# Kernel optimization log

Hardware: AMD Instinct MI355X
Metric: run time of the kernel (lower is better)

## Reference

```python
import jax, jax.numpy as jnp
import numpy as np

B, N_C, N_T, D, DF = 16, 2048, 1024, 2, 2
K, E_OBS = 16, 4
H, DH = 4, 16
F = H * DH  # 64-dim node features (embed_all output)


def setup_inputs() -> dict:
    key = jax.random.key(0)
    ks = jax.random.split(key, 16)
    r = lambda i, shape: jax.random.normal(ks[i], shape, jnp.float32) * 0.05
    d_in = E_OBS + D + DF  # obs(4) + s(2) + f(2) = 8
    return dict(
        s_ctx=jax.random.normal(ks[0], (B, N_C, D), jnp.float32),
        f_ctx=jax.random.normal(ks[1], (B, N_C, DF), jnp.float32),
        s_test=jax.random.normal(ks[2], (B, N_T, D), jnp.float32),
        emb_obs=r(3, (2, E_OBS)),
        W1=r(4, (d_in, 256)), b1=jnp.zeros((256,), jnp.float32),
        W2=r(5, (256, 128)), b2=jnp.zeros((128,), jnp.float32),
        W3=r(6, (128, F)), b3=jnp.zeros((F,), jnp.float32),
        ln_g=jnp.ones((F,), jnp.float32), ln_b=jnp.zeros((F,), jnp.float32),
        Wg=r(7, (F, F)),
        a_src=r(8, (H, DH)), a_dst=r(9, (H, DH)),
        We=r(10, (D, H)), be=jnp.zeros((H,), jnp.float32),
        H1=r(11, (F, 256)), c1=jnp.zeros((256,), jnp.float32),
        H2=r(12, (256, 64)), c2=jnp.zeros((64,), jnp.float32),
        H3=r(13, (64, 2)), c3=jnp.zeros((2,), jnp.float32),
    )


def _knn(q, ctx, k):
    # q [B,Nq,D], ctx [B,Nc,D] -> neighbor indices [B,Nq,K] and displacement edge feats [B,Nq,K,D]
    d2 = (jnp.sum(q * q, -1)[:, :, None] + jnp.sum(ctx * ctx, -1)[:, None, :]
          - 2.0 * jnp.einsum('bqd,bcd->bqc', q, ctx))
    _, idx = jax.lax.top_k(-d2, k)
    nb = jax.vmap(lambda c, i: c[i])(ctx, idx)  # gather neighbor coords per batch
    return idx, q[:, :, None, :] - nb


def _mlp3(x, W1, b1, W2, b2, W3, b3):
    x = jax.nn.gelu(x @ W1 + b1)
    x = jax.nn.gelu(x @ W2 + b2)
    return x @ W3 + b3


def _ln(x, g, b):
    mu = jnp.mean(x, -1, keepdims=True)
    v = jnp.var(x, -1, keepdims=True)
    return (x - mu) * jax.lax.rsqrt(v + 1e-6) * g + b


def reference(s_ctx, f_ctx, s_test, emb_obs, W1, b1, W2, b2, W3, b3, ln_g, ln_b,
              Wg, a_src, a_dst, We, be, H1, c1, H2, c2, H3, c3):
    # --- build kNN graph (ctx->ctx and ctx->test edges, K per receiver) ---
    s_cc, d_cc = _knn(s_ctx, s_ctx, K)
    s_ct, d_ct = _knn(s_test, s_ctx, K)
    edges = jnp.concatenate([d_cc.reshape(-1, D), d_ct.reshape(-1, D)], axis=0)  # [E, D]
    off = (jnp.arange(B) * N_C)[:, None, None]
    senders = jnp.concatenate([(s_cc + off).reshape(-1), (s_ct + off).reshape(-1)])  # [E]
    # receivers == repeat(arange(N), K): edges are grouped K-per-node in node order.

    # --- node embedding: [obs_embed | s | f] -> MLP -> LayerNorm ---
    ctx_in = jnp.concatenate([jnp.broadcast_to(emb_obs[1], (B, N_C, E_OBS)), s_ctx, f_ctx], -1)
    test_in = jnp.concatenate([jnp.broadcast_to(emb_obs[0], (B, N_T, E_OBS)), s_test,
                               jnp.zeros((B, N_T, DF), s_test.dtype)], -1)
    n_ctx = _ln(_mlp3(ctx_in, W1, b1, W2, b2, W3, b3), ln_g, ln_b)
    n_test = _ln(_mlp3(test_in, W1, b1, W2, b2, W3, b3), ln_g, ln_b)
    nodes = jnp.concatenate([n_ctx.reshape(B * N_C, F), n_test.reshape(B * N_T, F)], 0)
    N = B * (N_C + N_T)

    # --- edge-biased GAT message passing (K incoming edges per node) ---
    xp = (nodes @ Wg).reshape(N, H, DH)
    msg = xp[senders].reshape(N, K, H, DH)  # gather sender features
    sc = (jnp.einsum('nkhd,hd->nkh', msg, a_src)
          + jnp.einsum('nhd,hd->nh', xp, a_dst)[:, None, :])
    sc = jax.nn.leaky_relu(sc, 0.2) + (edges @ We + be).reshape(N, K, H)  # edge bias
    alpha = jax.nn.softmax(sc, axis=1)  # softmax over the K neighbors
    out = jnp.einsum('nkh,nkhd->nhd', alpha, msg).reshape(N, F)
    nodes = nodes + out  # residual

    # --- head on test nodes + diagonal MVN output ---
    n_t = nodes[-B * N_T:].reshape(B, N_T, F)
    o = jax.nn.gelu(n_t @ H1 + c1)
    o = jax.nn.gelu(o @ H2 + c2)
    o = o @ H3 + c3  # [B, N_t, 2]
    mean = o[..., 0:1]
    scale = jax.nn.softplus(o[..., 1:2])
    return jnp.concatenate([mean, scale], -1)
```

## Files before the change

kernel.cpp:

```cpp
#include <hip/hip_runtime.h>
#include <math.h>

#define NB 16
#define NCTX 2048
#define NTEST 1024
#define NCTX_TOT (NB*NCTX)
#define NTEST_TOT (NB*NTEST)
#define NTOT (NCTX_TOT + NTEST_TOT)

typedef _Float16 half8 __attribute__((ext_vector_type(8)));
typedef _Float16 half4 __attribute__((ext_vector_type(4)));
typedef float f32x4 __attribute__((ext_vector_type(4)));

__device__ __forceinline__ float gelu_f(float x) {
  float x3 = x * x * x;
  float y = 0.7978845608028654f * fmaf(0.044715f, x3, x);
  float e = __expf(2.0f * y);
  float th = 1.0f - 2.0f * __builtin_amdgcn_rcpf(e + 1.0f);
  return 0.5f * x * (1.0f + th);
}

__device__ __forceinline__ void fma4(float4& a, float s, float4 w) {
  a.x = fmaf(s, w.x, a.x);
  a.y = fmaf(s, w.y, a.y);
  a.z = fmaf(s, w.z, a.z);
  a.w = fmaf(s, w.w, a.w);
}

__device__ __forceinline__ float4 ldg4(const float* p) {
  return *reinterpret_cast<const float4*>(p);
}

__device__ __forceinline__ unsigned fkey(float f) {
  unsigned u = __float_as_uint(f);
  return (u & 0x80000000u) ? ~u : (u ^ 0x80000000u);
}
__device__ __forceinline__ float unfkey(unsigned k) {
  return (k & 0x80000000u) ? __uint_as_float(k ^ 0x80000000u)
                           : __uint_as_float(~k);
}

__global__ __launch_bounds__(256, 3) void knn_prep_kernel(
    const float* __restrict__ s_ctx, const float* __restrict__ s_test,
    int* __restrict__ senders,
    const float* __restrict__ W1, const float* __restrict__ b1,
    const float* __restrict__ emb,
    const float* __restrict__ W2, const float* __restrict__ W3,
    const float* __restrict__ Wg,
    const float* __restrict__ H1, const float* __restrict__ H2,
    _Float16* __restrict__ W2P, _Float16* __restrict__ W3P,
    _Float16* __restrict__ WgP,
    _Float16* __restrict__ H1P, _Float16* __restrict__ H2P,
    float* __restrict__ ctype)
{
  __shared__ __align__(16) unsigned long long sk[4][128];
  const int blk = blockIdx.x;

  if (blk < 40) {
    const int t = blk*256 + (int)threadIdx.x;
    if (t < 4096) {
      int i = t;
      int j = i >> 9, ks = (i >> 6) & 7, l = i & 63;
      int col = 16*j + (l & 15);
      int k0  = ks*32 + (l >> 4)*8;
      half8 o;
      #pragma unroll
      for (int e = 0; e < 8; ++e) o[e] = (_Float16)W2[(k0 + e)*128 + col];
      *reinterpret_cast<half8*>(&W2P[(size_t)i*8]) = o;
    } else if (t < 5120) {
      int i = t - 4096;
      int j = i >> 8, ks = (i >> 6) & 3, l = i & 63;
      int col = 16*j + (l & 15);
      int k0  = ks*32 + (l >> 4)*8;
      half8 o;
      #pragma unroll
      for (int e = 0; e < 8; ++e) o[e] = (_Float16)W3[(k0 + e)*64 + col];
      *reinterpret_cast<half8*>(&W3P[(size_t)i*8]) = o;
    } else if (t < 5632) {
      int i = t - 5120;
      int j = i >> 7, ks = (i >> 6) & 1, l = i & 63;
      int col = 16*j + (l & 15);
      int k0  = ks*32 + (l >> 4)*8;
      half8 o;
      #pragma unroll
      for (int e = 0; e < 8; ++e) o[e] = (_Float16)Wg[(k0 + e)*64 + col];
      *reinterpret_cast<half8*>(&WgP[(size_t)i*8]) = o;
    } else if (t < 7680) {
      int i = t - 5632;
      int j = i >> 7, ks = (i >> 6) & 1, l = i & 63;
      int col = 16*j + (l & 15);
      int k0  = ks*32 + (l >> 4)*8;
      half8 o;
      #pragma unroll
      for (int e = 0; e < 8; ++e) o[e] = (_Float16)H1[(k0 + e)*256 + col];
      *reinterpret_cast<half8*>(&H1P[(size_t)i*8]) = o;
    } else if (t < 9728) {
      int i = t - 7680;
      int j = i >> 9, ks = (i >> 6) & 7, l = i & 63;
      int col = 16*j + (l & 15);
      int k0  = ks*32 + (l >> 4)*8;
      half8 o;
      #pragma unroll
      for (int e = 0; e < 8; ++e) o[e] = (_Float16)H2[(k0 + e)*64 + col];
      *reinterpret_cast<half8*>(&H2P[(size_t)i*8]) = o;
    } else {
      int i = t - 9728;
      int ty = i >> 8, c = i & 255;
      float acc = b1[c];
      #pragma unroll
      for (int k = 0; k < 4; ++k) acc = fmaf(emb[ty*4 + k], W1[k*256 + c], acc);
      ctype[i] = acc;
    }
    return;
  }

  const int t    = threadIdx.x;
  const int lane = t & 63;
  const int w    = t >> 6;
  const int b0   = blk - 40;
  const int unit = (b0 & 7)*512 + (b0 >> 3);
  const int bb   = unit >> 8;
  const int q    = (unit & 255) * 4 + w;
  const int trow = bb * NTEST + q;

  const float* cb = s_ctx + (size_t)bb * NCTX * 2;
  const float qx = s_test[(size_t)trow*2];
  const float qy = s_test[(size_t)trow*2 + 1];
  const float qq = __fadd_rn(__fmul_rn(qx,qx), __fmul_rn(qy,qy));

  float2 p[32];
  #pragma unroll
  for (int it = 0; it < 32; ++it)
    p[it] = *reinterpret_cast<const float2*>(&cb[2*(it*64 + lane)]);

  float d[32];
  float mn = 3.4e38f;
  #pragma unroll
  for (int it = 0; it < 32; ++it) {
    float ss  = __fadd_rn(__fmul_rn(p[it].x,p[it].x), __fmul_rn(p[it].y,p[it].y));
    float dot = __fadd_rn(__fmul_rn(qx, p[it].x), __fmul_rn(qy, p[it].y));
    float d2  = __fsub_rn(__fadd_rn(qq, ss), __fmul_rn(2.0f, dot));
    d[it] = d2;
    mn = fminf(mn, d2);
  }

  unsigned v = fkey(mn);
  #pragma unroll
  for (int k = 2; k <= 64; k <<= 1) {
    #pragma unroll
    for (int j = k >> 1; j >= 1; j >>= 1) {
      unsigned pv = (unsigned)__shfl_xor((int)v, j);
      bool up      = ((lane & k) == 0);
      bool lowHalf = ((lane & j) == 0);
      bool keepMin = (lowHalf == up);
      unsigned mnv = v < pv ? v : pv;
      unsigned mxv = v < pv ? pv : v;
      v = keepMin ? mnv : mxv;
    }
  }
  const float Tf = unfkey((unsigned)__shfl((int)v, 15));

  int cnt = 0;
  #pragma unroll
  for (int it = 0; it < 32; ++it) cnt += (int)(d[it] <= Tf);
  int inc = cnt;
  #pragma unroll
  for (int o = 1; o < 64; o <<= 1) {
    int y = __shfl_up(inc, o);
    if (lane >= o) inc += y;
  }
  const int S = __shfl(inc, 63);
  int pos = inc - cnt;
  #pragma unroll
  for (int it = 0; it < 32; ++it) {
    if (d[it] <= Tf) {
      if (pos < 128)
        sk[w][pos] = ((unsigned long long)fkey(d[it]) << 32)
                   | (unsigned)(it*64 + lane);
      ++pos;
    }
  }

  if (S <= 32) {
    if (lane >= S && lane < 32) sk[w][lane] = ~0ULL;
    unsigned long long pm = sk[w][lane & 31];
    unsigned long long kv[32];
    #pragma unroll
    for (int j = 0; j < 32; ++j) kv[j] = sk[w][j];
    int r0 = 0;
    #pragma unroll
    for (int j = 0; j < 32; ++j)
      r0 += (int)(kv[j] < pm);
    if (lane < S && r0 < 16)
      senders[(size_t)trow*16 + r0] = bb*NCTX + (int)(pm & 0xFFFFFFFFu);
  } else if (S <= 128) {
    unsigned long long p0 = (lane      < S) ? sk[w][lane]      : ~0ULL;
    unsigned long long p1 = (lane + 64 < S) ? sk[w][lane + 64] : ~0ULL;
    int r0 = 0, r1 = 0;
    for (int j = 0; j < S; ++j) {
      unsigned long long kj = sk[w][j];
      r0 += (int)(kj < p0);
      r1 += (int)(kj < p1);
    }
    if (lane < S && r0 < 16)
      senders[(size_t)trow*16 + r0] = bb*NCTX + (int)(p0 & 0xFFFFFFFFu);
    if (lane + 64 < S && r1 < 16)
      senders[(size_t)trow*16 + r1] = bb*NCTX + (int)(p1 & 0xFFFFFFFFu);
  } else {
    if (lane == 0) {
      float dist[16]; int ind[16];
      #pragma unroll
      for (int j=0;j<16;++j){ dist[j]=3.4e38f; ind[j]=0; }
      for (int c = 0; c < NCTX; ++c) {
        float2 pp = *reinterpret_cast<const float2*>(&cb[2*c]);
        float ss  = __fadd_rn(__fmul_rn(pp.x,pp.x), __fmul_rn(pp.y,pp.y));
        float dot = __fadd_rn(__fmul_rn(qx, pp.x), __fmul_rn(qy, pp.y));
        float d2  = __fsub_rn(__fadd_rn(qq, ss), __fmul_rn(2.0f, dot));
        if (d2 < dist[15]) {
          float dj = d2; int ij = c;
          #pragma unroll
          for (int j = 0; j < 16; ++j) {
            bool sw = dj < dist[j];
            float td = dist[j]; int ti = ind[j];
            dist[j] = sw ? dj : td;  ind[j] = sw ? ij : ti;
            dj = sw ? td : dj;       ij = sw ? ti : ij;
          }
        }
      }
      for (int j = 0; j < 16; ++j)
        senders[(size_t)trow*16 + j] = bb*NCTX + ind[j];
    }
  }
}

__global__ __launch_bounds__(256, 4) void mlp_kernel(
    const float* __restrict__ s_ctx, const float* __restrict__ f_ctx,
    const float* __restrict__ s_test,
    const float* __restrict__ ctype, const float* __restrict__ W1,
    const _Float16* __restrict__ W2P, const float* __restrict__ b2,
    const _Float16* __restrict__ W3P, const float* __restrict__ b3,
    const float* __restrict__ ln_g, const float* __restrict__ ln_b,
    const _Float16* __restrict__ WgP,
    const float* __restrict__ a_src, const float* __restrict__ a_dst,
    float* __restrict__ nodes, _Float16* __restrict__ xph,
    float* __restrict__ xps, float* __restrict__ xpd)
{
  __shared__ __align__(16) char smem[34816];
  const int t    = threadIdx.x;
  const int lane = t & 63;
  const int w    = t >> 6;
  const int id   = blockIdx.x;
  char* slice = smem + w * 8704;
  _Float16* h1t  = reinterpret_cast<_Float16*>(slice);
  float (*xin)[4] = reinterpret_cast<float(*)[4]>(slice + 8448);
  _Float16* h2   = h1t;
  _Float16* nodh = h1t + 16*136;
  const int cn = lane & 15;
  const int kg = lane >> 4;
  const int m0 = (id*4 + w) * 16;
  const bool is_ctx = (m0 < NCTX_TOT);

  const _Float16* bQ2 = W2P + lane*8;
  const _Float16* bQ3 = W3P + lane*8;
  const _Float16* bQg = WgP + lane*8;

  half8 bb2[8];
  #pragma unroll
  for (int j = 0; j < 8; ++j)
    bb2[j] = *reinterpret_cast<const half8*>(bQ2 + j*4096);

  {
    int r = lane >> 2, c = lane & 3;
    int n = m0 + r;
    float v;
    if (is_ctx) v = (c < 2) ? s_ctx[2*(size_t)n + c] : f_ctx[2*(size_t)n + (c-2)];
    else { int tn = n - NCTX_TOT; v = (c < 2) ? s_test[2*(size_t)tn + c] : 0.f; }
    xin[r][c] = v;
  }

  {
    const int c0 = lane * 4;
    float4 w4 = ldg4(&W1[4*256 + c0]);
    float4 w5 = ldg4(&W1[5*256 + c0]);
    float4 w6 = ldg4(&W1[6*256 + c0]);
    float4 w7 = ldg4(&W1[7*256 + c0]);
    float4 cbv = ldg4(&ctype[(is_ctx ? 256 : 0) + c0]);
    #pragma unroll
    for (int r = 0; r < 16; ++r) {
      float4 xi = *reinterpret_cast<const float4*>(&xin[r][0]);
      float4 a = cbv;
      fma4(a, xi.x, w4); fma4(a, xi.y, w5);
      fma4(a, xi.z, w6); fma4(a, xi.w, w7);
      half4 o = { (_Float16)gelu_f(a.x), (_Float16)gelu_f(a.y),
                  (_Float16)gelu_f(a.z), (_Float16)gelu_f(a.w) };
      *reinterpret_cast<half4*>(&h1t[r*264 + c0]) = o;
    }
  }

  {
    f32x4 acc[8];
    #pragma unroll
    for (int j = 0; j < 8; ++j) {
      float bv = b2[16*j + cn];
      acc[j] = (f32x4){bv, bv, bv, bv};
    }
    const _Float16* aP = h1t + cn*264 + kg*8;
    #pragma unroll
    for (int ks = 0; ks < 8; ++ks) {
      half8 a = *reinterpret_cast<const half8*>(aP + ks*32);
      half8 bn[8];
      if (ks < 7) {
        #pragma unroll
        for (int j = 0; j < 8; ++j)
          bn[j] = *reinterpret_cast<const half8*>(bQ2 + j*4096 + (ks+1)*512);
      }
      #pragma unroll
      for (int j = 0; j < 8; ++j)
        acc[j] = __builtin_amdgcn_mfma_f32_16x16x32_f16(a, bb2[j], acc[j], 0, 0, 0);
      if (ks < 7) {
        #pragma unroll
        for (int j = 0; j < 8; ++j) bb2[j] = bn[j];
      }
    }
    #pragma unroll
    for (int j = 0; j < 8; ++j)
      #pragma unroll
      for (int r = 0; r < 4; ++r) {
        int m = kg*4 + r;
        h2[m*136 + 16*j + cn] = (_Float16)gelu_f(acc[j][r]);
      }
  }

  {
    f32x4 acc[4];
    #pragma unroll
    for (int j = 0; j < 4; ++j) {
      float bv = b3[16*j + cn];
      acc[j] = (f32x4){bv, bv, bv, bv};
    }
    const _Float16* aP = h2 + cn*136 + kg*8;
    half8 bb[4];
    #pragma unroll
    for (int j = 0; j < 4; ++j)
      bb[j] = *reinterpret_cast<const half8*>(bQ3 + j*2048);
    #pragma unroll
    for (int ks = 0; ks < 4; ++ks) {
      half8 a = *reinterpret_cast<const half8*>(aP + ks*32);
      half8 bn[4];
      if (ks < 3) {
        #pragma unroll
        for (int j = 0; j < 4; ++j)
          bn[j] = *reinterpret_cast<const half8*>(bQ3 + j*2048 + (ks+1)*512);
      }
      #pragma unroll
      for (int j = 0; j < 4; ++j)
        acc[j] = __builtin_amdgcn_mfma_f32_16x16x32_f16(a, bb[j], acc[j], 0, 0, 0);
      if (ks < 3) {
        #pragma unroll
        for (int j = 0; j < 4; ++j) bb[j] = bn[j];
      }
    }
    float gv[4], bvv[4];
    #pragma unroll
    for (int j = 0; j < 4; ++j) { gv[j] = ln_g[16*j+cn]; bvv[j] = ln_b[16*j+cn]; }
    const bool is_test = !is_ctx;
    #pragma unroll
    for (int r = 0; r < 4; ++r) {
      float sv = 0.f, sq = 0.f;
      #pragma unroll
      for (int j = 0; j < 4; ++j) {
        float v = acc[j][r];
        sv += v; sq += v*v;
      }
      #pragma unroll
      for (int o = 1; o < 16; o <<= 1) {
        sv += __shfl_xor(sv, o);
        sq += __shfl_xor(sq, o);
      }
      float mean = sv * (1.0f/64.0f);
      float var  = sq * (1.0f/64.0f) - mean*mean;
      float rstd = rsqrtf(var + 1e-6f);
      int m = kg*4 + r;
      #pragma unroll
      for (int j = 0; j < 4; ++j) {
        float v = (acc[j][r] - mean) * rstd * gv[j] + bvv[j];
        nodh[m*72 + 16*j + cn] = (_Float16)v;
        if (is_test)
          nodes[(size_t)(m0 + m)*64 + 16*j + cn] = v;
      }
    }
  }

  {
    f32x4 acc[4];
    #pragma unroll
    for (int j = 0; j < 4; ++j) acc[j] = (f32x4){0.f, 0.f, 0.f, 0.f};
    const _Float16* aP = nodh + cn*72 + kg*8;
    half8 bg0[4], bg1[4];
    #pragma unroll
    for (int j = 0; j < 4; ++j) {
      bg0[j] = *reinterpret_cast<const half8*>(bQg + j*1024);
      bg1[j] = *reinterpret_cast<const half8*>(bQg + j*1024 + 512);
    }
    half8 a0 = *reinterpret_cast<const half8*>(aP);
    half8 a1 = *reinterpret_cast<const half8*>(aP + 32);
    #pragma unroll
    for (int j = 0; j < 4; ++j)
      acc[j] = __builtin_amdgcn_mfma_f32_16x16x32_f16(a0, bg0[j], acc[j], 0, 0, 0);
    #pragma unroll
    for (int j = 0; j < 4; ++j)
      acc[j] = __builtin_amdgcn_mfma_f32_16x16x32_f16(a1, bg1[j], acc[j], 0, 0, 0);
    #pragma unroll
    for (int r = 0; r < 4; ++r) {
      int m = kg*4 + r;
      #pragma unroll
      for (int j = 0; j < 4; ++j)
        xph[(size_t)(m0 + m)*64 + 16*j + cn] = (_Float16)acc[j][r];
    }
    const float* av = is_ctx ? a_src : a_dst;
    float av0 = av[cn], av1 = av[16+cn], av2 = av[32+cn], av3 = av[48+cn];
    #pragma unroll
    for (int r = 0; r < 4; ++r) {
      float p0 = acc[0][r]*av0, p1 = acc[1][r]*av1;
      float p2 = acc[2][r]*av2, p3 = acc[3][r]*av3;
      #pragma unroll
      for (int o = 1; o < 16; o <<= 1) {
        p0 += __shfl_xor(p0, o); p1 += __shfl_xor(p1, o);
        p2 += __shfl_xor(p2, o); p3 += __shfl_xor(p3, o);
      }
      if (cn == 0) {
        int m = kg*4 + r;
        float4 v = make_float4(p0, p1, p2, p3);
        if (is_ctx)
          *reinterpret_cast<float4*>(&xps[(size_t)(m0 + m)*4]) = v;
        else
          *reinterpret_cast<float4*>(&xpd[(size_t)(m0 + m - NCTX_TOT)*4]) = v;
      }
    }
  }
}

__global__ __launch_bounds__(64, 3) void back_kernel(
    const float* __restrict__ s_ctx, const float* __restrict__ s_test,
    const _Float16* __restrict__ xph, const int* __restrict__ senders,
    const float* __restrict__ xps, const float* __restrict__ xpd,
    const float* __restrict__ We, const float* __restrict__ be,
    const float* __restrict__ nodes,
    const _Float16* __restrict__ H1P, const float* __restrict__ c1,
    const _Float16* __restrict__ H2P, const float* __restrict__ c2,
    const float* __restrict__ H3, const float* __restrict__ c3,
    float* __restrict__ outp)
{
  __shared__ __align__(16) _Float16 xinh[16*72];
  __shared__ __align__(16) _Float16 h1[16*264];
  const int lane = threadIdx.x;
  const int cn   = lane & 15;
  const int kg   = lane >> 4;
  const int bid  = blockIdx.x;
  const int L    = (bid & 7)*256 + (bid >> 3);
  const int row0 = L * 8;

  #pragma unroll
  for (int rr = 8; rr < 16; ++rr) xinh[rr*72 + lane] = (_Float16)0.f;

  {
    const int h  = kg;
    const int kk = cn;
    const int hb = lane & 48;
    const float we0 = We[h], we1 = We[4+h], beh = be[h];
    for (int rr = 0; rr < 8; ++rr) {
      const int trow = row0 + rr;
      int s = senders[(size_t)trow*16 + kk];
      s = (s < 0) ? 0 : ((s >= NCTX_TOT) ? NCTX_TOT - 1 : s);
      float pre = xps[(size_t)s*4 + h] + xpd[(size_t)trow*4 + h];
      float lr  = pre >= 0.f ? pre : 0.2f * pre;
      const float qx = s_test[(size_t)trow*2];
      const float qy = s_test[(size_t)trow*2 + 1];
      float ex = qx - s_ctx[(size_t)s*2];
      float ey = qy - s_ctx[(size_t)s*2 + 1];
      float sc = lr + fmaf(ex, we0, fmaf(ey, we1, beh));
      float mx = sc;
      #pragma unroll
      for (int o = 1; o < 16; o <<= 1) mx = fmaxf(mx, __shfl_xor(mx, o));
      float e = __expf(sc - mx);
      float sum = e;
      #pragma unroll
      for (int o = 1; o < 16; o <<= 1) sum += __shfl_xor(sum, o);
      float alpha = e / sum;
      float outv = 0.f;
      #pragma unroll
      for (int k = 0; k < 16; ++k) {
        int   sk = __shfl(s, k);
        float al = __shfl(alpha, hb + k);
        outv = fmaf(al, (float)xph[(size_t)sk*64 + lane], outv);
      }
      float xv = nodes[(size_t)(NCTX_TOT + trow)*64 + lane] + outv;
      xinh[rr*72 + lane] = (_Float16)xv;
    }
  }

  {
    const _Float16* aP  = xinh + cn*72 + kg*8;
    const _Float16* bQ1 = H1P + lane*8;
    half8 a0 = *reinterpret_cast<const half8*>(aP);
    half8 a1 = *reinterpret_cast<const half8*>(aP + 32);
    #pragma unroll
    for (int g = 0; g < 2; ++g) {
      f32x4 acc[8];
      #pragma unroll
      for (int j = 0; j < 8; ++j) {
        float bv = c1[16*(g*8 + j) + cn];
        acc[j] = (f32x4){bv, bv, bv, bv};
      }
      half8 b0[8], b1[8];
      #pragma unroll
      for (int j = 0; j < 8; ++j) {
        b0[j] = *reinterpret_cast<const half8*>(bQ1 + ((g*8 + j)*2 + 0)*512);
        b1[j] = *reinterpret_cast<const half8*>(bQ1 + ((g*8 + j)*2 + 1)*512);
      }
      #pragma unroll
      for (int j = 0; j < 8; ++j)
        acc[j] = __builtin_amdgcn_mfma_f32_16x16x32_f16(a0, b0[j], acc[j], 0, 0, 0);
      #pragma unroll
      for (int j = 0; j < 8; ++j)
        acc[j] = __builtin_amdgcn_mfma_f32_16x16x32_f16(a1, b1[j], acc[j], 0, 0, 0);
      #pragma unroll
      for (int j = 0; j < 8; ++j)
        #pragma unroll
        for (int r = 0; r < 4; ++r)
          h1[(kg*4 + r)*264 + 16*(g*8 + j) + cn] = (_Float16)gelu_f(acc[j][r]);
    }
  }

  {
    f32x4 acc[4];
    #pragma unroll
    for (int j = 0; j < 4; ++j) {
      float bv = c2[16*j + cn];
      acc[j] = (f32x4){bv, bv, bv, bv};
    }
    const _Float16* aP  = h1 + cn*264 + kg*8;
    const _Float16* bQ2 = H2P + lane*8;
    half8 bb[4];
    #pragma unroll
    for (int j = 0; j < 4; ++j)
      bb[j] = *reinterpret_cast<const half8*>(bQ2 + j*4096);
    #pragma unroll
    for (int ks = 0; ks < 8; ++ks) {
      half8 a = *reinterpret_cast<const half8*>(aP + ks*32);
      half8 bn[4];
      if (ks < 7) {
        #pragma unroll
        for (int j = 0; j < 4; ++j)
          bn[j] = *reinterpret_cast<const half8*>(bQ2 + j*4096 + (ks+1)*512);
      }
      #pragma unroll
      for (int j = 0; j < 4; ++j)
        acc[j] = __builtin_amdgcn_mfma_f32_16x16x32_f16(a, bb[j], acc[j], 0, 0, 0);
      if (ks < 7) {
        #pragma unroll
        for (int j = 0; j < 4; ++j) bb[j] = bn[j];
      }
    }
    float h30[4], h31[4];
    #pragma unroll
    for (int j = 0; j < 4; ++j) {
      h30[j] = H3[(16*j + cn)*2 + 0];
      h31[j] = H3[(16*j + cn)*2 + 1];
    }
    const float c30 = c3[0], c31 = c3[1];
    #pragma unroll
    for (int r = 0; r < 4; ++r) {
      float p0 = 0.f, p1 = 0.f;
      #pragma unroll
      for (int j = 0; j < 4; ++j) {
        float g = gelu_f(acc[j][r]);
        p0 = fmaf(g, h30[j], p0);
        p1 = fmaf(g, h31[j], p1);
      }
      #pragma unroll
      for (int o = 1; o < 16; o <<= 1) {
        p0 += __shfl_xor(p0, o);
        p1 += __shfl_xor(p1, o);
      }
      if (cn == 0 && kg < 2) {
        int row = row0 + kg*4 + r;
        float m = p0 + c30;
        float sa = p1 + c31;
        float sv = fmaxf(sa, 0.f) + log1pf(__expf(-fabsf(sa)));
        outp[(size_t)row*2 + 0] = m;
        outp[(size_t)row*2 + 1] = sv;
      }
    }
  }
}

extern "C" void kernel_launch(void* const* d_in, const int* in_sizes, int n_in,
                              void* d_out, int out_size, void* d_ws, size_t ws_size,
                              hipStream_t stream) {
  const float* s_ctx  = (const float*)d_in[0];
  const float* f_ctx  = (const float*)d_in[1];
  const float* s_test = (const float*)d_in[2];
  const float* emb    = (const float*)d_in[3];
  const float* W1 = (const float*)d_in[4];
  const float* b1 = (const float*)d_in[5];
  const float* W2 = (const float*)d_in[6];
  const float* b2 = (const float*)d_in[7];
  const float* W3 = (const float*)d_in[8];
  const float* b3 = (const float*)d_in[9];
  const float* ln_g = (const float*)d_in[10];
  const float* ln_b = (const float*)d_in[11];
  const float* Wg = (const float*)d_in[12];
  const float* a_src = (const float*)d_in[13];
  const float* a_dst = (const float*)d_in[14];
  const float* We = (const float*)d_in[15];
  const float* be = (const float*)d_in[16];
  const float* H1 = (const float*)d_in[17];
  const float* c1 = (const float*)d_in[18];
  const float* H2 = (const float*)d_in[19];
  const float* c2 = (const float*)d_in[20];
  const float* H3 = (const float*)d_in[21];
  const float* c3 = (const float*)d_in[22];

  float* nodes   = (float*)d_ws;
  _Float16* xph  = (_Float16*)(nodes + (size_t)NTOT*64);
  int*   senders = (int*)(xph + (size_t)NTOT*64);
  _Float16* W2P  = (_Float16*)(senders + (size_t)NTEST_TOT*16);
  _Float16* W3P  = W2P + 32768;
  _Float16* WgP  = W3P + 8192;
  _Float16* H1P  = WgP + 4096;
  _Float16* H2P  = H1P + 16384;
  float*   ctype = (float*)(H2P + 16384);
  float*   xps   = ctype + 512;
  float*   xpd   = xps + (size_t)NCTX_TOT*4;
  float* outp    = (float*)d_out;

  hipLaunchKernelGGL(knn_prep_kernel, dim3(4136), dim3(256), 0, stream,
                     s_ctx, s_test, senders,
                     W1, b1, emb, W2, W3, Wg, H1, H2,
                     W2P, W3P, WgP, H1P, H2P, ctype);
  hipLaunchKernelGGL(mlp_kernel, dim3(768), dim3(256), 0, stream,
                     s_ctx, f_ctx, s_test, ctype, W1,
                     W2P, b2, W3P, b3, ln_g, ln_b, WgP,
                     a_src, a_dst, nodes, xph, xps, xpd);
  hipLaunchKernelGGL(back_kernel, dim3(2048), dim3(64), 0, stream,
                     s_ctx, s_test, xph, senders, xps, xpd, We, be,
                     nodes, H1P, c1, H2P, c2, H3, c3, outp);
}
```

Baseline: 71.56 us.

## Split back_kernel head across two waves with 16 real rows per block

Result: faster. 64.07 us (-10.5%).

```diff
diff --git a/kernel.cpp b/kernel.cpp
--- a/kernel.cpp
+++ b/kernel.cpp
@@ -440,7 +440,7 @@
   }
 }
 
-__global__ __launch_bounds__(64, 3) void back_kernel(
+__global__ __launch_bounds__(128, 3) void back_kernel(
     const float* __restrict__ s_ctx, const float* __restrict__ s_test,
     const _Float16* __restrict__ xph, const int* __restrict__ senders,
     const float* __restrict__ xps, const float* __restrict__ xpd,
@@ -453,15 +453,15 @@
 {
   __shared__ __align__(16) _Float16 xinh[16*72];
   __shared__ __align__(16) _Float16 h1[16*264];
-  const int lane = threadIdx.x;
+  __shared__ float pp[2][16][2];
+  const int tid  = threadIdx.x;
+  const int lane = tid & 63;
+  const int wv   = tid >> 6;
   const int cn   = lane & 15;
   const int kg   = lane >> 4;
   const int bid  = blockIdx.x;
-  const int L    = (bid & 7)*256 + (bid >> 3);
-  const int row0 = L * 8;
-
-  #pragma unroll
-  for (int rr = 8; rr < 16; ++rr) xinh[rr*72 + lane] = (_Float16)0.f;
+  const int L    = (bid & 7)*128 + (bid >> 3);
+  const int row0 = L * 16;
 
   {
     const int h  = kg;
@@ -469,7 +469,8 @@
     const int hb = lane & 48;
     const float we0 = We[h], we1 = We[4+h], beh = be[h];
     for (int rr = 0; rr < 8; ++rr) {
-      const int trow = row0 + rr;
+      const int rl   = wv*8 + rr;
+      const int trow = row0 + rl;
       int s = senders[(size_t)trow*16 + kk];
       s = (s < 0) ? 0 : ((s >= NCTX_TOT) ? NCTX_TOT - 1 : s);
       float pre = xps[(size_t)s*4 + h] + xpd[(size_t)trow*4 + h];
@@ -495,103 +496,114 @@
         outv = fmaf(al, (float)xph[(size_t)sk*64 + lane], outv);
       }
       float xv = nodes[(size_t)(NCTX_TOT + trow)*64 + lane] + outv;
-      xinh[rr*72 + lane] = (_Float16)xv;
-    }
-  }
+      xinh[rl*72 + lane] = (_Float16)xv;
+    }
+  }
+
+  __syncthreads();
 
   {
     const _Float16* aP  = xinh + cn*72 + kg*8;
     const _Float16* bQ1 = H1P + lane*8;
     half8 a0 = *reinterpret_cast<const half8*>(aP);
     half8 a1 = *reinterpret_cast<const half8*>(aP + 32);
-    #pragma unroll
-    for (int g = 0; g < 2; ++g) {
-      f32x4 acc[8];
-      #pragma unroll
-      for (int j = 0; j < 8; ++j) {
-        float bv = c1[16*(g*8 + j) + cn];
-        acc[j] = (f32x4){bv, bv, bv, bv};
-      }
-      half8 b0[8], b1[8];
-      #pragma unroll
-      for (int j = 0; j < 8; ++j) {
-        b0[j] = *reinterpret_cast<const half8*>(bQ1 + ((g*8 + j)*2 + 0)*512);
-        b1[j] = *reinterpret_cast<const half8*>(bQ1 + ((g*8 + j)*2 + 1)*512);
-      }
-      #pragma unroll
-      for (int j = 0; j < 8; ++j)
-        acc[j] = __builtin_amdgcn_mfma_f32_16x16x32_f16(a0, b0[j], acc[j], 0, 0, 0);
-      #pragma unroll
-      for (int j = 0; j < 8; ++j)
-        acc[j] = __builtin_amdgcn_mfma_f32_16x16x32_f16(a1, b1[j], acc[j], 0, 0, 0);
-      #pragma unroll
-      for (int j = 0; j < 8; ++j)
-        #pragma unroll
-        for (int r = 0; r < 4; ++r)
-          h1[(kg*4 + r)*264 + 16*(g*8 + j) + cn] = (_Float16)gelu_f(acc[j][r]);
-    }
-  }
-
-  {
-    f32x4 acc[4];
-    #pragma unroll
-    for (int j = 0; j < 4; ++j) {
+    const int g = wv;
+    f32x4 acc[8];
+    #pragma unroll
+    for (int j = 0; j < 8; ++j) {
+      float bv = c1[16*(g*8 + j) + cn];
+      acc[j] = (f32x4){bv, bv, bv, bv};
+    }
+    half8 b0[8], b1[8];
+    #pragma unroll
+    for (int j = 0; j < 8; ++j) {
+      b0[j] = *reinterpret_cast<const half8*>(bQ1 + ((g*8 + j)*2 + 0)*512);
+      b1[j] = *reinterpret_cast<const half8*>(bQ1 + ((g*8 + j)*2 + 1)*512);
+    }
+    #pragma unroll
+    for (int j = 0; j < 8; ++j)
+      acc[j] = __builtin_amdgcn_mfma_f32_16x16x32_f16(a0, b0[j], acc[j], 0, 0, 0);
+    #pragma unroll
+    for (int j = 0; j < 8; ++j)
+      acc[j] = __builtin_amdgcn_mfma_f32_16x16x32_f16(a1, b1[j], acc[j], 0, 0, 0);
+    #pragma unroll
+    for (int j = 0; j < 8; ++j)
+      #pragma unroll
+      for (int r = 0; r < 4; ++r)
+        h1[(kg*4 + r)*264 + 16*(g*8 + j) + cn] = (_Float16)gelu_f(acc[j][r]);
+  }
+
+  __syncthreads();
+
+  {
+    f32x4 acc[2];
+    #pragma unroll
+    for (int j2 = 0; j2 < 2; ++j2) {
+      const int j = wv*2 + j2;
       float bv = c2[16*j + cn];
-      acc[j] = (f32x4){bv, bv, bv, bv};
+      acc[j2] = (f32x4){bv, bv, bv, bv};
     }
     const _Float16* aP  = h1 + cn*264 + kg*8;
     const _Float16* bQ2 = H2P + lane*8;
-    half8 bb[4];
-    #pragma unroll
-    for (int j = 0; j < 4; ++j)
-      bb[j] = *reinterpret_cast<const half8*>(bQ2 + j*4096);
+    half8 bb[2];
+    #pragma unroll
+    for (int j2 = 0; j2 < 2; ++j2)
+      bb[j2] = *reinterpret_cast<const half8*>(bQ2 + (wv*2 + j2)*4096);
     #pragma unroll
     for (int ks = 0; ks < 8; ++ks) {
       half8 a = *reinterpret_cast<const half8*>(aP + ks*32);
-      half8 bn[4];
+      half8 bn[2];
       if (ks < 7) {
         #pragma unroll
-        for (int j = 0; j < 4; ++j)
-          bn[j] = *reinterpret_cast<const half8*>(bQ2 + j*4096 + (ks+1)*512);
-      }
-      #pragma unroll
-      for (int j = 0; j < 4; ++j)
-        acc[j] = __builtin_amdgcn_mfma_f32_16x16x32_f16(a, bb[j], acc[j], 0, 0, 0);
+        for (int j2 = 0; j2 < 2; ++j2)
+          bn[j2] = *reinterpret_cast<const half8*>(bQ2 + (wv*2 + j2)*4096 + (ks+1)*512);
+      }
+      #pragma unroll
+      for (int j2 = 0; j2 < 2; ++j2)
+        acc[j2] = __builtin_amdgcn_mfma_f32_16x16x32_f16(a, bb[j2], acc[j2], 0, 0, 0);
       if (ks < 7) {
         #pragma unroll
-        for (int j = 0; j < 4; ++j) bb[j] = bn[j];
-      }
-    }
-    float h30[4], h31[4];
-    #pragma unroll
-    for (int j = 0; j < 4; ++j) {
-      h30[j] = H3[(16*j + cn)*2 + 0];
-      h31[j] = H3[(16*j + cn)*2 + 1];
-    }
-    const float c30 = c3[0], c31 = c3[1];
+        for (int j2 = 0; j2 < 2; ++j2) bb[j2] = bn[j2];
+      }
+    }
+    float h30[2], h31[2];
+    #pragma unroll
+    for (int j2 = 0; j2 < 2; ++j2) {
+      const int j = wv*2 + j2;
+      h30[j2] = H3[(16*j + cn)*2 + 0];
+      h31[j2] = H3[(16*j + cn)*2 + 1];
+    }
     #pragma unroll
     for (int r = 0; r < 4; ++r) {
       float p0 = 0.f, p1 = 0.f;
       #pragma unroll
-      for (int j = 0; j < 4; ++j) {
-        float g = gelu_f(acc[j][r]);
-        p0 = fmaf(g, h30[j], p0);
-        p1 = fmaf(g, h31[j], p1);
+      for (int j2 = 0; j2 < 2; ++j2) {
+        float g = gelu_f(acc[j2][r]);
+        p0 = fmaf(g, h30[j2], p0);
+        p1 = fmaf(g, h31[j2], p1);
       }
       #pragma unroll
       for (int o = 1; o < 16; o <<= 1) {
         p0 += __shfl_xor(p0, o);
         p1 += __shfl_xor(p1, o);
       }
-      if (cn == 0 && kg < 2) {
-        int row = row0 + kg*4 + r;
-        float m = p0 + c30;
-        float sa = p1 + c31;
-        float sv = fmaxf(sa, 0.f) + log1pf(__expf(-fabsf(sa)));
-        outp[(size_t)row*2 + 0] = m;
-        outp[(size_t)row*2 + 1] = sv;
-      }
-    }
+      if (cn == 0) {
+        pp[wv][kg*4 + r][0] = p0;
+        pp[wv][kg*4 + r][1] = p1;
+      }
+    }
+  }
+
+  __syncthreads();
+
+  if (wv == 0 && lane < 16) {
+    const float c30 = c3[0], c31 = c3[1];
+    float m  = pp[0][lane][0] + pp[1][lane][0] + c30;
+    float sa = pp[0][lane][1] + pp[1][lane][1] + c31;
+    float sv = fmaxf(sa, 0.f) + log1pf(__expf(-fabsf(sa)));
+    int row = row0 + lane;
+    outp[(size_t)row*2 + 0] = m;
+    outp[(size_t)row*2 + 1] = sv;
   }
 }
 
@@ -643,7 +655,7 @@
                      s_ctx, f_ctx, s_test, ctype, W1,
                      W2P, b2, W3P, b3, ln_g, ln_b, WgP,
                      a_src, a_dst, nodes, xph, xps, xpd);
-  hipLaunchKernelGGL(back_kernel, dim3(2048), dim3(64), 0, stream,
+  hipLaunchKernelGGL(back_kernel, dim3(1024), dim3(128), 0, stream,
                      s_ctx, s_test, xph, senders, xps, xpd, We, be,
                      nodes, H1P, c1, H2P, c2, H3, c3, outp);
 }
```
